# Kernel optimization log

Measured on AMD Instinct MI355X. Metric: run time of the kernel, lower is better.

Reference implementation:

```python
import jax, jax.numpy as jnp
import numpy as np

IN_DIM = 768
N_HEADS = 12
HEAD_DIM = IN_DIM // N_HEADS


def setup_inputs() -> dict:
    key = jax.random.key(0)
    k1, k2, k3, k4, k5 = jax.random.split(key, 5)
    x = jax.random.normal(k1, (2, 2048, IN_DIM), dtype=jnp.float32)
    s = 1.0 / np.sqrt(IN_DIM)
    W_qkv = jax.random.uniform(k2, (IN_DIM, 3 * IN_DIM), jnp.float32, -s, s)
    b_qkv = jax.random.uniform(k3, (3 * IN_DIM,), jnp.float32, -s, s)
    W_out = jax.random.uniform(k4, (IN_DIM, IN_DIM), jnp.float32, -s, s)
    b_out = jax.random.uniform(k5, (IN_DIM,), jnp.float32, -s, s)
    return {"x": x, "W_qkv": W_qkv, "b_qkv": b_qkv, "W_out": W_out, "b_out": b_out}


def reference(x, W_qkv, b_qkv, W_out, b_out):
    B, N, D = x.shape
    qkv = x @ W_qkv + b_qkv  # [B, N, 3D]
    qkv = qkv.reshape(B, N, 3, N_HEADS, HEAD_DIM)
    qkv = jnp.transpose(qkv, (2, 0, 3, 1, 4))  # [3, B, H, N, Dh]
    q, k, v = qkv[0], qkv[1], qkv[2]
    scale = 1.0 / np.sqrt(HEAD_DIM)
    scores = jnp.einsum("bhqd,bhkd->bhqk", q, k) * scale  # [B, H, N, N]
    attn = jax.nn.softmax(scores, axis=-1)
    out = jnp.einsum("bhqk,bhkd->bhqd", attn, v)  # [B, H, N, Dh]
    out = jnp.transpose(out, (0, 2, 1, 3)).reshape(B, N, D)
    return out @ W_out + b_out
```

## Files before the change

kernel.cpp:

```cpp
#include <hip/hip_runtime.h>

#define DEVI __device__ __forceinline__

typedef __attribute__((ext_vector_type(8))) short short8;
typedef __attribute__((ext_vector_type(4))) float f32x4;

DEVI unsigned short f32_to_bf16(float f) {
  unsigned int u = __float_as_uint(f);
  u += 0x7fffu + ((u >> 16) & 1u);
  return (unsigned short)(u >> 16);
}
DEVI float bf16_to_f32(unsigned short h) {
  return __uint_as_float(((unsigned int)h) << 16);
}

DEVI void gld_lds16(const void* g, void* l) {
  __builtin_amdgcn_global_load_lds(
      (__attribute__((address_space(1))) void*)(g),
      (__attribute__((address_space(3))) void*)(l), 16, 0, 0);
}

__global__ void k_cast_bf16(const float* __restrict__ in, unsigned short* __restrict__ out,
                            int total8) {
  int i = blockIdx.x * blockDim.x + threadIdx.x;
  if (i >= total8) return;
  const float* src = in + i * 8;
  short8 v;
#pragma unroll
  for (int j = 0; j < 8; ++j) v[j] = (short)f32_to_bf16(src[j]);
  *(short8*)&out[(size_t)i * 8] = v;
}

__global__ __launch_bounds__(256) void k_cast_Bt(const float* __restrict__ W,
                                                 unsigned short* __restrict__ Wt,
                                                 int K, int N) {
  int kt = blockIdx.x, nt = blockIdx.y;
  __shared__ float t[32][33];
  int tid = threadIdx.x;
#pragma unroll
  for (int p = 0; p < 4; ++p) {
    int idx = tid + p * 256;
    int rr = idx >> 5, cc = idx & 31;
    t[rr][cc] = W[(size_t)(kt * 32 + rr) * N + nt * 32 + cc];
  }
  __syncthreads();
#pragma unroll
  for (int p = 0; p < 4; ++p) {
    int idx = tid + p * 256;
    int rn = idx >> 5, ck = idx & 31;
    Wt[(size_t)(nt * 32 + rn) * K + kt * 32 + ck] = f32_to_bf16(t[ck][rn]);
  }
}

__global__ __launch_bounds__(256) void k_gemm_qkv(const unsigned short* __restrict__ A,
                                                  const unsigned short* __restrict__ Bt,
                                                  const float* __restrict__ bias,
                                                  int M, int N, int K,
                                                  unsigned short* __restrict__ Qo,
                                                  unsigned short* __restrict__ Ko,
                                                  unsigned short* __restrict__ Vo) {
  __shared__ __align__(16) unsigned short As[128 * 32];
  __shared__ __align__(16) unsigned short Bs[128 * 32];
  int tid = threadIdx.x;
  int tm = blockIdx.x, tn = blockIdx.y;
  int lane = tid & 63, wid = tid >> 6;
  int wr = wid >> 1, wc = wid & 1;
  int g = lane >> 4, lr = lane & 15;
  f32x4 acc[4][4] = {};
  int srow = tid >> 2;
  int scol = (tid & 3) * 8;
  const unsigned short* Ab = A + (size_t)tm * 128 * K;
  const unsigned short* Bb = Bt + (size_t)tn * 128 * K;
  for (int k0 = 0; k0 < K; k0 += 32) {
    gld_lds16(Ab + (size_t)srow * K + k0 + scol, &As[srow * 32 + scol]);
    gld_lds16(Ab + (size_t)(srow + 64) * K + k0 + scol, &As[(srow + 64) * 32 + scol]);
    gld_lds16(Bb + (size_t)srow * K + k0 + scol, &Bs[srow * 32 + scol]);
    gld_lds16(Bb + (size_t)(srow + 64) * K + k0 + scol, &Bs[(srow + 64) * 32 + scol]);
    __syncthreads();
    short8 a[4], b[4];
#pragma unroll
    for (int m = 0; m < 4; ++m)
      a[m] = *(const short8*)&As[(wr * 64 + m * 16 + lr) * 32 + g * 8];
#pragma unroll
    for (int n = 0; n < 4; ++n)
      b[n] = *(const short8*)&Bs[(wc * 64 + n * 16 + lr) * 32 + g * 8];
#pragma unroll
    for (int m = 0; m < 4; ++m)
#pragma unroll
      for (int n = 0; n < 4; ++n)
        acc[m][n] = __builtin_amdgcn_mfma_f32_16x16x32_bf16(a[m], b[n], acc[m][n], 0, 0, 0);
    __syncthreads();
  }
#pragma unroll
  for (int m = 0; m < 4; ++m) {
#pragma unroll
    for (int n = 0; n < 4; ++n) {
      int col = tn * 128 + wc * 64 + n * 16 + lr;
      float bv = bias[col];
      int sec = (col >= 1536) ? 2 : ((col >= 768) ? 1 : 0);
      int c = col - sec * 768;
      int hh = c >> 6, d = c & 63;
#pragma unroll
      for (int j = 0; j < 4; ++j) {
        int row = tm * 128 + wr * 64 + m * 16 + g * 4 + j;
        int bb = row >> 11, nn = row & 2047;
        size_t dst = (((size_t)(bb * 12 + hh) << 11) + nn) * 64 + d;
        unsigned short hv = f32_to_bf16(acc[m][n][j] + bv);
        if (sec == 0)
          Qo[dst] = hv;
        else if (sec == 1)
          Ko[dst] = hv;
        else
          Vo[dst] = hv;
      }
    }
  }
}

__global__ __launch_bounds__(256) void k_gemm2(const unsigned short* __restrict__ A,
                                               const unsigned short* __restrict__ Bt,
                                               const float* __restrict__ bias,
                                               float* __restrict__ C,
                                               int M, int N, int K) {
  __shared__ __align__(16) unsigned short As[64 * 32];
  __shared__ __align__(16) unsigned short Bs[128 * 32];
  int tid = threadIdx.x;
  int tm = blockIdx.x, tn = blockIdx.y;
  int lane = tid & 63, wid = tid >> 6;
  int wr = wid >> 1, wc = wid & 1;
  int g = lane >> 4, lr = lane & 15;
  f32x4 acc[2][4] = {};
  int srow = tid >> 2;
  int scol = (tid & 3) * 8;
  const unsigned short* Ab = A + (size_t)tm * 64 * K;
  const unsigned short* Bb = Bt + (size_t)tn * 128 * K;
  for (int k0 = 0; k0 < K; k0 += 32) {
    gld_lds16(Ab + (size_t)srow * K + k0 + scol, &As[srow * 32 + scol]);
    gld_lds16(Bb + (size_t)srow * K + k0 + scol, &Bs[srow * 32 + scol]);
    gld_lds16(Bb + (size_t)(srow + 64) * K + k0 + scol, &Bs[(srow + 64) * 32 + scol]);
    __syncthreads();
    short8 a[2], b[4];
#pragma unroll
    for (int m = 0; m < 2; ++m)
      a[m] = *(const short8*)&As[(wr * 32 + m * 16 + lr) * 32 + g * 8];
#pragma unroll
    for (int n = 0; n < 4; ++n)
      b[n] = *(const short8*)&Bs[(wc * 64 + n * 16 + lr) * 32 + g * 8];
#pragma unroll
    for (int m = 0; m < 2; ++m)
#pragma unroll
      for (int n = 0; n < 4; ++n)
        acc[m][n] = __builtin_amdgcn_mfma_f32_16x16x32_bf16(a[m], b[n], acc[m][n], 0, 0, 0);
    __syncthreads();
  }
#pragma unroll
  for (int m = 0; m < 2; ++m) {
#pragma unroll
    for (int n = 0; n < 4; ++n) {
      int col = tn * 128 + wc * 64 + n * 16 + lr;
      float bv = bias[col];
#pragma unroll
      for (int j = 0; j < 4; ++j) {
        int row = tm * 64 + wr * 32 + m * 16 + g * 4 + j;
        C[(size_t)row * N + col] = acc[m][n][j] + bv;
      }
    }
  }
}

__global__ __launch_bounds__(256) void k_v_transpose(const unsigned short* __restrict__ Vc,
                                                     unsigned short* __restrict__ Vt) {
  int bh = blockIdx.x;
  int nt = blockIdx.y;
  __shared__ unsigned short s[64][65];
  int tid = threadIdx.x;
  int r = tid >> 2;
#pragma unroll
  for (int p = 0; p < 2; ++p) {
    int c = (tid & 3) + p * 4;
    short8 v = *(const short8*)&Vc[((size_t)(bh * 2048 + nt * 64 + r)) * 64 + c * 8];
#pragma unroll
    for (int ii = 0; ii < 8; ++ii) s[r][c * 8 + ii] = (unsigned short)v[ii];
  }
  __syncthreads();
  int d = tid >> 2;
#pragma unroll
  for (int p = 0; p < 2; ++p) {
    int c = (tid & 3) + p * 4;
    short8 w;
#pragma unroll
    for (int ii = 0; ii < 8; ++ii) w[ii] = (short)s[c * 8 + ii][d];
    *(short8*)&Vt[((size_t)bh * 64 + d) * 2048 + nt * 64 + c * 8] = w;
  }
}


#define ATTN_STAGE(KSB, VSB, T)                                                          \
  {                                                                                      \
    int kv0 = (T) * 64;                                                                  \
    _Pragma("unroll") for (int it = 0; it < 2; ++it) {                                   \
      int L = tid + it * 256;                                                            \
      int rw = L >> 3, s7 = L & 7;                                                       \
      gld_lds16(Kb + (size_t)(khead + kv0 + rw) * 64 + ((s7 ^ (rw & 7)) * 8),            \
                &KSB[L * 8]);                                                            \
      gld_lds16(Vt + (size_t)(vhead + rw) * 2048 + kv0 + ((s7 ^ (rw & 7)) * 8),          \
                &VSB[L * 8]);                                                            \
    }                                                                                    \
  }

#define PROC_TILE(KSB, VSB)                                                              \
  {                                                                                      \
    f32x4 s[4];                                                                          \
    _Pragma("unroll") for (int m = 0; m < 4; ++m) {                                      \
      short8 kf0 = *(const short8*)&KSB[(m * 16 + lr) * 64 + ((g ^ (lr & 7)) * 8)];      \
      short8 kf1 =                                                                       \
          *(const short8*)&KSB[(m * 16 + lr) * 64 + (((g + 4) ^ (lr & 7)) * 8)];         \
      f32x4 z = {0.f, 0.f, 0.f, 0.f};                                                    \
      z = __builtin_amdgcn_mfma_f32_16x16x32_bf16(kf0, qf0, z, 0, 0, 0);                 \
      s[m] = __builtin_amdgcn_mfma_f32_16x16x32_bf16(kf1, qf1, z, 0, 0, 0);              \
    }                                                                                    \
    _Pragma("unroll") for (int m = 0; m < 4; ++m) {                                      \
      _Pragma("unroll") for (int j = 0; j < 4; ++j) {                                    \
        float pv = exp2f(__builtin_fmaf(s[m][j], C, -8.0f));                             \
        s[m][j] = pv;                                                                    \
        lrun += pv;                                                                      \
      }                                                                                  \
    }                                                                                    \
    _Pragma("unroll") for (int m = 0; m < 4; ++m) {                                      \
      unsigned int d0, d1;                                                               \
      asm("v_cvt_pk_bf16_f32 %0, %1, %2" : "=v"(d0) : "v"(s[m][0]), "v"(s[m][1]));       \
      asm("v_cvt_pk_bf16_f32 %0, %1, %2" : "=v"(d1) : "v"(s[m][2]), "v"(s[m][3]));       \
      uint2 w;                                                                           \
      w.x = d0;                                                                          \
      w.y = d1;                                                                          \
      *(uint2*)&Ps[wid][lr * 64 + (((m * 2 + (g >> 1)) ^ lr) & 7) * 8 + (g & 1) * 4] =   \
          w;                                                                             \
    }                                                                                    \
    _Pragma("unroll") for (int kk = 0; kk < 2; ++kk) {                                   \
      short8 pa = *(const short8*)&Ps[wid][lr * 64 + (((kk * 4 + g) ^ lr) & 7) * 8];     \
      _Pragma("unroll") for (int nt = 0; nt < 4; ++nt) {                                 \
        short8 vb =                                                                      \
            *(const short8*)&VSB[(nt * 16 + lr) * 64 + (((kk * 4 + g) ^ (lr & 7)) & 7) * \
                                                           8];                           \
        oacc[nt] = __builtin_amdgcn_mfma_f32_16x16x32_bf16(pa, vb, oacc[nt], 0, 0, 0);   \
      }                                                                                  \
    }                                                                                    \
  }

__global__ __launch_bounds__(256, 4) void k_attn(const unsigned short* __restrict__ Qb,
                                                 const unsigned short* __restrict__ Kb,
                                                 const unsigned short* __restrict__ Vt,
                                                 unsigned short* __restrict__ Xh) {
  int bh = blockIdx.x;
  int qb = blockIdx.y;
  int b = bh / 12, h = bh - b * 12;
  __shared__ __align__(16) unsigned short Ks0[64 * 64], Ks1[64 * 64];
  __shared__ __align__(16) unsigned short Vs0[64 * 64], Vs1[64 * 64];
  __shared__ __align__(16) unsigned short Ps[4][16 * 64];
  int tid = threadIdx.x;
  int wid = tid >> 6, lane = tid & 63;
  int g = lane >> 4, lr = lane & 15;
  const float C = 0.125f * 1.4426950408889634f;
  int khead = bh * 2048;
  int vhead = bh * 64;
  int q0 = qb * 64 + wid * 16;

  short8 qf0 = *(const short8*)&Qb[(size_t)(khead + q0 + lr) * 64 + g * 8];
  short8 qf1 = *(const short8*)&Qb[(size_t)(khead + q0 + lr) * 64 + 32 + g * 8];

  float lrun = 0.f;
  f32x4 oacc[4] = {};

  ATTN_STAGE(Ks0, Vs0, 0);
  __syncthreads();
#pragma unroll 1
  for (int tt = 0; tt < 16; ++tt) {
    ATTN_STAGE(Ks1, Vs1, 2 * tt + 1);
    PROC_TILE(Ks0, Vs0);
    __syncthreads();
    if (tt < 15) ATTN_STAGE(Ks0, Vs0, 2 * tt + 2);
    PROC_TILE(Ks1, Vs1);
    __syncthreads();
  }

  lrun += __shfl_xor(lrun, 16, 64);
  lrun += __shfl_xor(lrun, 32, 64);
  float linv = 1.0f / lrun;
  float lf[4];
#pragma unroll
  for (int j = 0; j < 4; ++j) lf[j] = __shfl(linv, g * 4 + j, 64);
#pragma unroll
  for (int nt = 0; nt < 4; ++nt)
#pragma unroll
    for (int j = 0; j < 4; ++j) {
      int row = b * 2048 + q0 + g * 4 + j;
      int col = h * 64 + nt * 16 + lr;
      Xh[(size_t)row * 768 + col] = f32_to_bf16(oacc[nt][j] * lf[j]);
    }
}

extern "C" void kernel_launch(void* const* d_in, const int* in_sizes, int n_in,
                              void* d_out, int out_size, void* d_ws, size_t ws_size,
                              hipStream_t stream) {
  const float* x = (const float*)d_in[0];
  const float* W_qkv = (const float*)d_in[1];
  const float* b_qkv = (const float*)d_in[2];
  const float* W_out = (const float*)d_in[3];
  const float* b_out = (const float*)d_in[4];
  float* out = (float*)d_out;
  char* ws = (char*)d_ws;

  unsigned short* Xh = (unsigned short*)(ws + 0);
  unsigned short* Xb = (unsigned short*)(ws + 18874368);
  unsigned short* Wq_t = (unsigned short*)(ws + 25165824);
  unsigned short* Wo_t = (unsigned short*)(ws + 28704768);
  unsigned short* Qb = (unsigned short*)(ws + 32243712);
  unsigned short* Kb = (unsigned short*)(ws + 38535168);
  unsigned short* Vc = (unsigned short*)(ws + 44826624);
  unsigned short* Vt = (unsigned short*)(ws + 51118080);

  k_cast_bf16<<<(4096 * 768 / 8 + 255) / 256, 256, 0, stream>>>(x, Xb, 4096 * 768 / 8);
  k_cast_Bt<<<dim3(24, 72), 256, 0, stream>>>(W_qkv, Wq_t, 768, 2304);
  k_cast_Bt<<<dim3(24, 24), 256, 0, stream>>>(W_out, Wo_t, 768, 768);
  k_gemm_qkv<<<dim3(32, 18), 256, 0, stream>>>(Xb, Wq_t, b_qkv, 4096, 2304, 768, Qb, Kb, Vc);
  k_v_transpose<<<dim3(24, 32), 256, 0, stream>>>(Vc, Vt);
  k_attn<<<dim3(24, 32), 256, 0, stream>>>(Qb, Kb, Vt, Xh);
  k_gemm2<<<dim3(64, 6), 256, 0, stream>>>(Xh, Wo_t, b_out, out, 4096, 768, 768);
}
```

Measured before the change: 110.9 us.

## Fold softmax scale into Q, retile output GEMM, interleave PV with P writes

Premultiplies Q by the softmax scale (in log2 units) in the QKV GEMM epilogue, so attention calls exp2 directly on raw scores and drops the per-element FMA and the fixed -8 offset. Shrinks the output projection GEMM tile to 64x64 and doubles the grid to raise occupancy and wave count. Splits the P-to-LDS writes and PV MFMAs into interleaved halves and wraps the MFMA sections in s_setprio. Removing the offset risks exp2 overflow for large scores, and rounding the scaled Q to bf16 changes precision slightly.

Result: no change. 110.9 us (-0.0%).

```diff
diff --git a/kernel.cpp b/kernel.cpp
--- a/kernel.cpp
+++ b/kernel.cpp
@@ -91,6 +91,7 @@
         acc[m][n] = __builtin_amdgcn_mfma_f32_16x16x32_bf16(a[m], b[n], acc[m][n], 0, 0, 0);
     __syncthreads();
   }
+  const float QSCALE = 0.125f * 1.4426950408889634f;
 #pragma unroll
   for (int m = 0; m < 4; ++m) {
 #pragma unroll
@@ -105,13 +106,14 @@
         int row = tm * 128 + wr * 64 + m * 16 + g * 4 + j;
         int bb = row >> 11, nn = row & 2047;
         size_t dst = (((size_t)(bb * 12 + hh) << 11) + nn) * 64 + d;
-        unsigned short hv = f32_to_bf16(acc[m][n][j] + bv);
-        if (sec == 0)
-          Qo[dst] = hv;
-        else if (sec == 1)
-          Ko[dst] = hv;
-        else
-          Vo[dst] = hv;
+        float outv = acc[m][n][j] + bv;
+        if (sec == 0) {
+          Qo[dst] = f32_to_bf16(outv * QSCALE);
+        } else if (sec == 1) {
+          Ko[dst] = f32_to_bf16(outv);
+        } else {
+          Vo[dst] = f32_to_bf16(outv);
+        }
       }
     }
   }
@@ -123,41 +125,40 @@
                                                float* __restrict__ C,
                                                int M, int N, int K) {
   __shared__ __align__(16) unsigned short As[64 * 32];
-  __shared__ __align__(16) unsigned short Bs[128 * 32];
+  __shared__ __align__(16) unsigned short Bs[64 * 32];
   int tid = threadIdx.x;
   int tm = blockIdx.x, tn = blockIdx.y;
   int lane = tid & 63, wid = tid >> 6;
   int wr = wid >> 1, wc = wid & 1;
   int g = lane >> 4, lr = lane & 15;
-  f32x4 acc[2][4] = {};
+  f32x4 acc[2][2] = {};
   int srow = tid >> 2;
   int scol = (tid & 3) * 8;
   const unsigned short* Ab = A + (size_t)tm * 64 * K;
-  const unsigned short* Bb = Bt + (size_t)tn * 128 * K;
+  const unsigned short* Bb = Bt + (size_t)tn * 64 * K;
   for (int k0 = 0; k0 < K; k0 += 32) {
     gld_lds16(Ab + (size_t)srow * K + k0 + scol, &As[srow * 32 + scol]);
     gld_lds16(Bb + (size_t)srow * K + k0 + scol, &Bs[srow * 32 + scol]);
-    gld_lds16(Bb + (size_t)(srow + 64) * K + k0 + scol, &Bs[(srow + 64) * 32 + scol]);
-    __syncthreads();
-    short8 a[2], b[4];
+    __syncthreads();
+    short8 a[2], b[2];
 #pragma unroll
     for (int m = 0; m < 2; ++m)
       a[m] = *(const short8*)&As[(wr * 32 + m * 16 + lr) * 32 + g * 8];
 #pragma unroll
-    for (int n = 0; n < 4; ++n)
-      b[n] = *(const short8*)&Bs[(wc * 64 + n * 16 + lr) * 32 + g * 8];
+    for (int n = 0; n < 2; ++n)
+      b[n] = *(const short8*)&Bs[(wc * 32 + n * 16 + lr) * 32 + g * 8];
 #pragma unroll
     for (int m = 0; m < 2; ++m)
 #pragma unroll
-      for (int n = 0; n < 4; ++n)
+      for (int n = 0; n < 2; ++n)
         acc[m][n] = __builtin_amdgcn_mfma_f32_16x16x32_bf16(a[m], b[n], acc[m][n], 0, 0, 0);
     __syncthreads();
   }
 #pragma unroll
   for (int m = 0; m < 2; ++m) {
 #pragma unroll
-    for (int n = 0; n < 4; ++n) {
-      int col = tn * 128 + wc * 64 + n * 16 + lr;
+    for (int n = 0; n < 2; ++n) {
+      int col = tn * 64 + wc * 32 + n * 16 + lr;
       float bv = bias[col];
 #pragma unroll
       for (int j = 0; j < 4; ++j) {
@@ -208,9 +209,33 @@
     }                                                                                    \
   }
 
+#define PS_WRITE(M)                                                                      \
+  {                                                                                      \
+    unsigned int d0, d1;                                                                 \
+    asm("v_cvt_pk_bf16_f32 %0, %1, %2" : "=v"(d0) : "v"(s[M][0]), "v"(s[M][1]));         \
+    asm("v_cvt_pk_bf16_f32 %0, %1, %2" : "=v"(d1) : "v"(s[M][2]), "v"(s[M][3]));         \
+    uint2 w;                                                                             \
+    w.x = d0;                                                                            \
+    w.y = d1;                                                                            \
+    *(uint2*)&Ps[wid][lr * 64 + ((((M)*2 + (g >> 1)) ^ lr) & 7) * 8 + (g & 1) * 4] = w;  \
+  }
+
+#define PV_KK(KK, VSB)                                                                   \
+  {                                                                                      \
+    short8 pa = *(const short8*)&Ps[wid][lr * 64 + ((((KK)*4 + g) ^ lr) & 7) * 8];       \
+    __builtin_amdgcn_s_setprio(1);                                                       \
+    _Pragma("unroll") for (int nt = 0; nt < 4; ++nt) {                                   \
+      short8 vb = *(const short8*)&VSB[(nt * 16 + lr) * 64 +                             \
+                                       ((((KK)*4 + g) ^ (lr & 7)) & 7) * 8];             \
+      oacc[nt] = __builtin_amdgcn_mfma_f32_16x16x32_bf16(pa, vb, oacc[nt], 0, 0, 0);     \
+    }                                                                                    \
+    __builtin_amdgcn_s_setprio(0);                                                       \
+  }
+
 #define PROC_TILE(KSB, VSB)                                                              \
   {                                                                                      \
     f32x4 s[4];                                                                          \
+    __builtin_amdgcn_s_setprio(1);                                                       \
     _Pragma("unroll") for (int m = 0; m < 4; ++m) {                                      \
       short8 kf0 = *(const short8*)&KSB[(m * 16 + lr) * 64 + ((g ^ (lr & 7)) * 8)];      \
       short8 kf1 =                                                                       \
@@ -219,32 +244,20 @@
       z = __builtin_amdgcn_mfma_f32_16x16x32_bf16(kf0, qf0, z, 0, 0, 0);                 \
       s[m] = __builtin_amdgcn_mfma_f32_16x16x32_bf16(kf1, qf1, z, 0, 0, 0);              \
     }                                                                                    \
+    __builtin_amdgcn_s_setprio(0);                                                       \
     _Pragma("unroll") for (int m = 0; m < 4; ++m) {                                      \
       _Pragma("unroll") for (int j = 0; j < 4; ++j) {                                    \
-        float pv = exp2f(__builtin_fmaf(s[m][j], C, -8.0f));                             \
+        float pv = exp2f(s[m][j]);                                                       \
         s[m][j] = pv;                                                                    \
         lrun += pv;                                                                      \
       }                                                                                  \
     }                                                                                    \
-    _Pragma("unroll") for (int m = 0; m < 4; ++m) {                                      \
-      unsigned int d0, d1;                                                               \
-      asm("v_cvt_pk_bf16_f32 %0, %1, %2" : "=v"(d0) : "v"(s[m][0]), "v"(s[m][1]));       \
-      asm("v_cvt_pk_bf16_f32 %0, %1, %2" : "=v"(d1) : "v"(s[m][2]), "v"(s[m][3]));       \
-      uint2 w;                                                                           \
-      w.x = d0;                                                                          \
-      w.y = d1;                                                                          \
-      *(uint2*)&Ps[wid][lr * 64 + (((m * 2 + (g >> 1)) ^ lr) & 7) * 8 + (g & 1) * 4] =   \
-          w;                                                                             \
-    }                                                                                    \
-    _Pragma("unroll") for (int kk = 0; kk < 2; ++kk) {                                   \
-      short8 pa = *(const short8*)&Ps[wid][lr * 64 + (((kk * 4 + g) ^ lr) & 7) * 8];     \
-      _Pragma("unroll") for (int nt = 0; nt < 4; ++nt) {                                 \
-        short8 vb =                                                                      \
-            *(const short8*)&VSB[(nt * 16 + lr) * 64 + (((kk * 4 + g) ^ (lr & 7)) & 7) * \
-                                                           8];                           \
-        oacc[nt] = __builtin_amdgcn_mfma_f32_16x16x32_bf16(pa, vb, oacc[nt], 0, 0, 0);   \
-      }                                                                                  \
-    }                                                                                    \
+    PS_WRITE(0)                                                                          \
+    PS_WRITE(1)                                                                          \
+    PV_KK(0, VSB)                                                                        \
+    PS_WRITE(2)                                                                          \
+    PS_WRITE(3)                                                                          \
+    PV_KK(1, VSB)                                                                        \
   }
 
 __global__ __launch_bounds__(256, 4) void k_attn(const unsigned short* __restrict__ Qb,
@@ -260,7 +273,6 @@
   int tid = threadIdx.x;
   int wid = tid >> 6, lane = tid & 63;
   int g = lane >> 4, lr = lane & 15;
-  const float C = 0.125f * 1.4426950408889634f;
   int khead = bh * 2048;
   int vhead = bh * 64;
   int q0 = qb * 64 + wid * 16;
@@ -325,5 +337,5 @@
   k_gemm_qkv<<<dim3(32, 18), 256, 0, stream>>>(Xb, Wq_t, b_qkv, 4096, 2304, 768, Qb, Kb, Vc);
   k_v_transpose<<<dim3(24, 32), 256, 0, stream>>>(Vc, Vt);
   k_attn<<<dim3(24, 32), 256, 0, stream>>>(Qb, Kb, Vt, Xh);
-  k_gemm2<<<dim3(64, 6), 256, 0, stream>>>(Xh, Wo_t, b_out, out, 4096, 768, 768);
-}
+  k_gemm2<<<dim3(64, 12), 256, 0, stream>>>(Xh, Wo_t, b_out, out, 4096, 768, 768);
+}
```
